# Kernel optimization log

Hardware: AMD Instinct MI355X
Metric: run time of the kernel (lower is better)

Reference implementation:

```python
import jax, jax.numpy as jnp
import numpy as np
import math

BS, T = 256, 128
DD, DT, DB = 128, 16, 32
DH, NH, DS = 256, 4, 64
DHN = DH * NH


def _lin(key, din, dout):
    kw, kb = jax.random.split(key)
    w = jax.random.normal(kw, (din, dout), jnp.float32) * 0.02
    bb = jax.random.normal(kb, (dout,), jnp.float32) * 0.02
    return w, bb


def setup_inputs() -> dict:
    key = jax.random.key(0)
    ks = jax.random.split(key, 16)
    inp = {
        "x": jax.random.normal(ks[0], (BS, T, DD), jnp.float32),
        "a": jax.random.normal(ks[1], (BS, T, DT), jnp.float32),
        "m": jnp.ones((BS, T, DD), jnp.float32),
        "b": jax.random.normal(ks[2], (BS, DB), jnp.float32),
        "eps": jax.random.normal(ks[3], (T - 1, BS, DS), jnp.float32),
    }
    inp["bk_w"], inp["bk_b"] = _lin(ks[4], DD + DB, DH)
    inp["bv_w"], inp["bv_b"] = _lin(ks[5], DD + DB, DHN)
    inp["q_w"], inp["q_b"] = _lin(ks[6], DD + DT, DHN)
    inp["v_w"], inp["v_b"] = _lin(ks[7], DD + DT, DHN)
    inp["hk_w"], inp["hk_b"] = _lin(ks[8], DS, DH)
    inp["hv_w"], inp["hv_b"] = _lin(ks[9], DS, DHN)
    inp["mu1_w"], inp["mu1_b"] = _lin(ks[10], DHN, DS)
    inp["sg1_w"], inp["sg1_b"] = _lin(ks[11], DHN, DS)
    inp["mut_w"], inp["mut_b"] = _lin(ks[12], DHN, DS)
    inp["sgt_w"], inp["sgt_b"] = _lin(ks[13], DHN, DS)
    return inp


def reference(x, a, m, b, eps,
              bk_w, bk_b, bv_w, bv_b, q_w, q_b, v_w, v_b,
              hk_w, hk_b, hv_w, hv_b,
              mu1_w, mu1_b, sg1_w, sg1_b, mut_w, mut_b, sgt_w, sgt_b):
    bs = x.shape[0]
    inp = jnp.concatenate([x[:, 1:, :], a[:, :-1, :]], -1)   # [bs, T-1, DD+DT]
    mask = (jnp.sum(m[:, 1:, :], -1) > 0.0).astype(x.dtype)  # [bs, T-1]

    q_inp = jax.nn.relu(inp @ q_w + q_b).reshape(bs, -1, DH, NH)  # [bs,T-1,DH,NH]
    v_inp = (inp @ v_w + v_b).reshape(bs, -1, DH, NH)

    scale = 1.0 / math.sqrt(DH)

    def attn(key_vec):  # key_vec: [bs, DH]
        scores = jnp.einsum('bd,btdh->bth', key_vec, q_inp) * scale
        scores = jnp.where(mask[..., None] > 0, scores, -1e9)
        p = jax.nn.softmax(scores, axis=1)                 # over time
        return jnp.einsum('bth,btdh->bdh', p, v_inp).reshape(bs, DHN)

    xb = jnp.concatenate([x[:, 0, :], b], -1)              # [bs, DD+DB]
    key1 = jax.nn.relu(xb @ bk_w + bk_b)
    val1 = xb @ bv_w + bv_b
    h1 = jax.nn.relu(0.5 * (attn(key1) + val1))
    mu1 = h1 @ mu1_w + mu1_b
    sg1 = jax.nn.softplus(h1 @ sg1_w + sg1_b)
    z1 = mu1 + sg1 * eps[0]

    def step(z_prev, e):
        keyt = jax.nn.relu(z_prev @ hk_w + hk_b)
        valt = z_prev @ hv_w + hv_b
        ht = jax.nn.relu(0.5 * (attn(keyt) + valt))
        mu = ht @ mut_w + mut_b
        sg = jax.nn.softplus(ht @ sgt_w + sgt_b)
        z = mu + sg * e
        return z, (z, mu, sg)

    _, (zs, mus, sgs) = jax.lax.scan(step, z1, eps[1:])
    Z = jnp.moveaxis(jnp.concatenate([z1[None], zs], 0), 0, 1)    # [bs, T-1, DS]
    MU = jnp.moveaxis(jnp.concatenate([mu1[None], mus], 0), 0, 1)
    SG = jnp.moveaxis(jnp.concatenate([sg1[None], sgs], 0), 0, 1)
    return Z, MU, SG
```

## Files before the change

### kernel.cpp

```cpp
#include <hip/hip_runtime.h>
#include <hip/hip_bf16.h>
#include <stdint.h>

#define BS   256
#define T_   128
#define TP   127
#define DD   128
#define DT   16
#define DB   32
#define DH   256
#define NH   4
#define DS   64
#define DHN  1024

#define OFFV (256u*127u*64u)

typedef __attribute__((ext_vector_type(8))) short short8v;
typedef __attribute__((ext_vector_type(4))) float f32x4;
typedef __attribute__((ext_vector_type(2))) unsigned int uint2v;

__device__ __forceinline__ float bf16lo(unsigned u){ return __uint_as_float(u << 16); }
__device__ __forceinline__ float bf16hi(unsigned u){ return __uint_as_float(u & 0xffff0000u); }
__device__ __forceinline__ unsigned short f2bf(float f){
  unsigned u = __float_as_uint(f);
  u += 0x7fffu + ((u >> 16) & 1u);
  return (unsigned short)(u >> 16);
}
__device__ __forceinline__ unsigned pk2(float lo, float hi){
  return (unsigned)f2bf(lo) | ((unsigned)f2bf(hi) << 16);
}
__device__ __forceinline__ float softplus_f(float x){
  return fmaxf(x, 0.f) + log1pf(__expf(-fabsf(x)));
}

__global__ __launch_bounds__(256) void pack_w_kernel(
    const float* __restrict__ hk_w, const float* __restrict__ hv_w,
    const float* __restrict__ mut_w, const float* __restrict__ sgt_w,
    unsigned* __restrict__ hkp, unsigned* __restrict__ hvp,
    unsigned* __restrict__ mutp, unsigned* __restrict__ sgtp)
{
  int i = blockIdx.x * 256 + threadIdx.x;
  if (i < 32*256) { int s2 = i >> 8, d = i & 255;
    hkp[i] = pk2(hk_w[(2*s2)*256 + d], hk_w[(2*s2+1)*256 + d]); }
  if (i < 32*1024) { int s2 = i >> 10, j = i & 1023;
    hvp[i] = pk2(hv_w[(2*s2)*1024 + j], hv_w[(2*s2+1)*1024 + j]); }
  if (i < 512*64) { int J2 = i >> 6, k = i & 63;
    mutp[i] = pk2(mut_w[(2*J2)*64 + k], mut_w[(2*J2+1)*64 + k]);
    sgtp[i] = pk2(sgt_w[(2*J2)*64 + k], sgt_w[(2*J2+1)*64 + k]); }
}

#define LDA 168

__global__ __launch_bounds__(256) void proj_kernel(
    const float* __restrict__ x, const float* __restrict__ a,
    const float* __restrict__ q_w, const float* __restrict__ q_b,
    const float* __restrict__ v_w, const float* __restrict__ v_b,
    uint2v* __restrict__ Qp4, unsigned* __restrict__ Vws)
{
  const int b    = blockIdx.x;
  const int tid  = threadIdx.x;
  const int lane = tid & 63;
  const int w    = tid >> 6;

  __shared__ __align__(16) unsigned short A_s[128 * LDA];
  __shared__ __align__(16) unsigned short BC_s[64 * LDA];

  for (int idx = tid; idx < 128 * DD; idx += 256) {
    int t = idx >> 7, k = idx & 127;
    float v = (t < TP) ? x[((size_t)b * T_ + 1 + t) * DD + k] : 0.f;
    A_s[t * LDA + k] = f2bf(v);
  }
  for (int idx = tid; idx < 128 * 40; idx += 256) {
    int t = idx / 40, kk = idx % 40;
    float v = (t < TP && kk < DT) ? a[((size_t)b * T_ + t) * DT + kk] : 0.f;
    A_s[t * LDA + 128 + kk] = f2bf(v);
  }
  __syncthreads();

  for (int nt = 0; nt < 32; ++nt) {
    const int n0 = nt * 64;
    const bool isQ = (n0 < DHN);
    const float* wsrc = isQ ? q_w : v_w;
    const float* bias = isQ ? q_b : v_b;
    const int nb = isQ ? n0 : (n0 - DHN);

    for (int idx = tid; idx < 160 * 64; idx += 256) {
      int k = idx >> 6, n = idx & 63;
      float v = (k < DD + DT) ? wsrc[(size_t)k * DHN + nb + n] : 0.f;
      BC_s[n * LDA + k] = f2bf(v);
    }
    __syncthreads();

    f32x4 acc[2][4];
#pragma unroll
    for (int mi = 0; mi < 2; ++mi)
#pragma unroll
      for (int ni = 0; ni < 4; ++ni) { f32x4 zz = {0.f,0.f,0.f,0.f}; acc[mi][ni] = zz; }
    const int mb = w * 32;
#pragma unroll
    for (int kc = 0; kc < 5; ++kc) {
      const int ko = kc * 32 + ((lane >> 4) << 3);
      short8v af[2], bf[4];
#pragma unroll
      for (int mi = 0; mi < 2; ++mi)
        af[mi] = *(const short8v*)&A_s[(mb + mi*16 + (lane & 15)) * LDA + ko];
#pragma unroll
      for (int ni = 0; ni < 4; ++ni)
        bf[ni] = *(const short8v*)&BC_s[(ni*16 + (lane & 15)) * LDA + ko];
#pragma unroll
      for (int mi = 0; mi < 2; ++mi)
#pragma unroll
        for (int ni = 0; ni < 4; ++ni)
          acc[mi][ni] = __builtin_amdgcn_mfma_f32_16x16x32_bf16(af[mi], bf[ni], acc[mi][ni], 0, 0, 0);
    }
    __syncthreads();

#pragma unroll
    for (int mi = 0; mi < 2; ++mi)
#pragma unroll
      for (int ni = 0; ni < 4; ++ni) {
        int cl = ni*16 + (lane & 15);
        float bb = bias[nb + cl];
#pragma unroll
        for (int q = 0; q < 4; ++q) {
          int t = mb + mi*16 + ((lane >> 4) << 2) + q;
          float vv = acc[mi][ni][q] + bb;
          if (isQ) vv = fmaxf(vv, 0.f);
          BC_s[t * 66 + cl] = f2bf(vv);
        }
      }
    __syncthreads();

    if (isQ) {
      for (int idx = tid; idx < 4 * 512; idx += 256) {
        int d4l = idx >> 9, r = idx & 511;
        int t = r >> 2, h = r & 3;
        const unsigned short* cr = &BC_s[t * 66 + d4l * 16 + h];
        uint2v u;
        u.x = (unsigned)cr[0] | ((unsigned)cr[4]  << 16);
        u.y = (unsigned)cr[8] | ((unsigned)cr[12] << 16);
        Qp4[((size_t)b * 64 + (n0 >> 4) + d4l) * 512 + r] = u;
      }
    } else {
      int c0 = (n0 - DHN) >> 1;
      for (int idx = tid; idx < 128 * 32; idx += 256) {
        int t = idx >> 5, c2 = idx & 31;
        const unsigned short* cr = &BC_s[t * 66 + c2 * 2];
        Vws[((size_t)b * 128 + t) * 512 + c0 + c2] = (unsigned)cr[0] | ((unsigned)cr[1] << 16);
      }
    }
    __syncthreads();
  }
}

__global__ __launch_bounds__(512) void recur_kernel(
    const float* __restrict__ x, const float* __restrict__ bvec,
    const float* __restrict__ m, const float* __restrict__ eps,
    const float* __restrict__ bk_w, const float* __restrict__ bk_b,
    const float* __restrict__ bv_w, const float* __restrict__ bv_b,
    const float* __restrict__ hk_b, const float* __restrict__ hv_b,
    const float* __restrict__ mu1_w, const float* __restrict__ mu1_b,
    const float* __restrict__ sg1_w, const float* __restrict__ sg1_b,
    const float* __restrict__ mut_b, const float* __restrict__ sgt_b,
    const unsigned* __restrict__ hkp, const unsigned* __restrict__ hvp,
    const unsigned* __restrict__ mutp, const unsigned* __restrict__ sgtp,
    const uint2v* __restrict__ Qp4, const unsigned* __restrict__ Vws,
    float* __restrict__ out)
{
  const int b    = blockIdx.x;
  const int tid  = threadIdx.x;
  const int lane = tid & 63;
  const int wv   = tid >> 6;

  __shared__ __align__(16) float key_s[DH];
  __shared__ __align__(16) float sc[512];
  __shared__ __align__(16) float p_s[128 * 4];
  __shared__ __align__(16) float val_s[DHN];
  __shared__ __align__(16) float ht_s[DHN];
  __shared__ __align__(16) float red[2 * 8 * 64];
  __shared__ __align__(16) float z_s[DS];
  __shared__ __align__(16) float xb[DD + DB];
  __shared__ float mask_s[128];
  __shared__ __align__(16) float hkb_s[DH];
  __shared__ __align__(16) float hvb_s[DHN];
  __shared__ float mtb_s[DS], stb_s[DS];

  if (tid < DD + DB) xb[tid] = (tid < DD) ? x[(size_t)b * T_ * DD + tid] : bvec[b * DB + (tid - DD)];
  if (tid >= 256 && tid < 512) hkb_s[tid - 256] = hk_b[tid - 256];
  for (int i = tid; i < DHN; i += 512) hvb_s[i] = hv_b[i];
  if (tid < DS) { mtb_s[tid] = mut_b[tid]; stb_s[tid] = sgt_b[tid]; }

  for (int t = wv; t < TP; t += 8) {
    const float* mr = m + ((size_t)b * T_ + 1 + t) * DD;
    float s = mr[lane] + mr[lane + 64];
    for (int o = 1; o < 64; o <<= 1) s += __shfl_xor(s, o);
    if (lane == 0) mask_s[t] = (s > 0.f) ? 1.f : 0.f;
  }
  if (tid == 0) mask_s[127] = 0.f;
  __syncthreads();

  const uint2v*   qp = Qp4 + (size_t)b * 64 * 512 + tid;
  const unsigned* vp = Vws + (size_t)b * 128 * 512 + tid;
  const int h0 = (tid & 1) * 2;

  auto attn_phase = [&]() {
    float acc0 = 0.f, acc1 = 0.f;
#pragma unroll 8
    for (int d4 = 0; d4 < 64; ++d4) {
      uint2v q = __builtin_nontemporal_load(qp + (size_t)d4 * 512);
      float4 kk = *(const float4*)&key_s[d4 * 4];
      acc0 = fmaf(bf16lo(q.x), kk.x, acc0);
      acc1 = fmaf(bf16hi(q.x), kk.y, acc1);
      acc0 = fmaf(bf16lo(q.y), kk.z, acc0);
      acc1 = fmaf(bf16hi(q.y), kk.w, acc1);
    }
    {
      int t = tid >> 2;
      float s = acc0 + acc1;
      sc[tid] = (mask_s[t] > 0.f) ? s * 0.0625f : -1e9f;
    }
    __syncthreads();
    if (tid < 256) {
      int h = wv, l = lane;
      float v1 = sc[l * 4 + h];
      float v2 = (l + 64 < TP) ? sc[(l + 64) * 4 + h] : -3.0e38f;
      float mm = fmaxf(v1, v2);
      for (int o = 1; o < 64; o <<= 1) mm = fmaxf(mm, __shfl_xor(mm, o));
      float e1 = __expf(v1 - mm);
      float e2 = (l + 64 < TP) ? __expf(v2 - mm) : 0.f;
      float ssum = e1 + e2;
      for (int o = 1; o < 64; o <<= 1) ssum += __shfl_xor(ssum, o);
      float inv = 1.f / ssum;
      p_s[l * 4 + h] = e1 * inv;
      if (l + 64 < TP) p_s[(l + 64) * 4 + h] = e2 * inv;
    }
    __syncthreads();
    float a0 = 0.f, a1 = 0.f;
#pragma unroll 4
    for (int t2 = 0; t2 < TP; ++t2) {
      unsigned v = __builtin_nontemporal_load(vp + (size_t)t2 * 512);
      float2 pp = *(const float2*)&p_s[t2 * 4 + h0];
      a0 = fmaf(pp.x, bf16lo(v), a0);
      a1 = fmaf(pp.y, bf16hi(v), a1);
    }
    int j = tid * 2;
    ht_s[j]     = fmaxf(0.5f * (a0 + val_s[j]), 0.f);
    ht_s[j + 1] = fmaxf(0.5f * (a1 + val_s[j + 1]), 0.f);
    __syncthreads();
  };

  if (tid < 256) {
    float acc = bk_b[tid];
    for (int s = 0; s < DD + DB; ++s) acc = fmaf(xb[s], bk_w[s * DH + tid], acc);
    key_s[tid] = fmaxf(acc, 0.f);
  } else {
    int c = tid - 256;
    float a0 = bv_b[c], a1 = bv_b[c + 256], a2 = bv_b[c + 512], a3 = bv_b[c + 768];
    for (int s = 0; s < DD + DB; ++s) {
      float xs = xb[s];
      const float* r = bv_w + (size_t)s * DHN + c;
      a0 = fmaf(xs, r[0], a0);   a1 = fmaf(xs, r[256], a1);
      a2 = fmaf(xs, r[512], a2); a3 = fmaf(xs, r[768], a3);
    }
    val_s[c] = a0; val_s[c + 256] = a1; val_s[c + 512] = a2; val_s[c + 768] = a3;
  }
  __syncthreads();

  attn_phase();

  {
    int k = tid & 63, g = tid >> 6;
    float am = 0.f, as_ = 0.f;
    for (int jl = 0; jl < 128; ++jl) {
      int j = g * 128 + jl;
      float hj = ht_s[j];
      am  = fmaf(hj, mu1_w[(size_t)j * 64 + k], am);
      as_ = fmaf(hj, sg1_w[(size_t)j * 64 + k], as_);
    }
    red[g * 64 + k] = am; red[512 + g * 64 + k] = as_;
  }
  __syncthreads();
  if (tid < 64) {
    float mu = mu1_b[tid], sl = sg1_b[tid];
    for (int g = 0; g < 8; ++g) { mu += red[g * 64 + tid]; sl += red[512 + g * 64 + tid]; }
    float sg = softplus_f(sl);
    float z  = fmaf(sg, eps[(size_t)b * 64 + tid], mu);
    size_t o0 = ((size_t)b * TP + 0) * 64 + tid;
    out[o0] = z; out[OFFV + o0] = mu; out[2ull * OFFV + o0] = sg;
    z_s[tid] = z;
  }
  __syncthreads();

  for (int st = 1; st < TP; ++st) {
    if (tid < 256) {
      float acc = hkb_s[tid];
#pragma unroll 8
      for (int s2 = 0; s2 < 32; ++s2) {
        unsigned wq = hkp[s2 * 256 + tid];
        float2 zz = *(const float2*)&z_s[s2 * 2];
        acc = fmaf(zz.x, bf16lo(wq), acc);
        acc = fmaf(zz.y, bf16hi(wq), acc);
      }
      key_s[tid] = fmaxf(acc, 0.f);
    } else {
      int c = tid - 256;
      float a0 = hvb_s[c], a1 = hvb_s[c + 256], a2 = hvb_s[c + 512], a3 = hvb_s[c + 768];
#pragma unroll 4
      for (int s2 = 0; s2 < 32; ++s2) {
        float2 zz = *(const float2*)&z_s[s2 * 2];
        unsigned w0 = hvp[s2 * 1024 + c];
        unsigned w1 = hvp[s2 * 1024 + c + 256];
        unsigned w2 = hvp[s2 * 1024 + c + 512];
        unsigned w3 = hvp[s2 * 1024 + c + 768];
        a0 = fmaf(zz.x, bf16lo(w0), a0); a0 = fmaf(zz.y, bf16hi(w0), a0);
        a1 = fmaf(zz.x, bf16lo(w1), a1); a1 = fmaf(zz.y, bf16hi(w1), a1);
        a2 = fmaf(zz.x, bf16lo(w2), a2); a2 = fmaf(zz.y, bf16hi(w2), a2);
        a3 = fmaf(zz.x, bf16lo(w3), a3); a3 = fmaf(zz.y, bf16hi(w3), a3);
      }
      val_s[c] = a0; val_s[c + 256] = a1; val_s[c + 512] = a2; val_s[c + 768] = a3;
    }
    __syncthreads();

    attn_phase();

    {
      int k = tid & 63, g = tid >> 6;
      float am0 = 0.f, am1 = 0.f, as0 = 0.f, as1 = 0.f;
#pragma unroll 4
      for (int j2 = 0; j2 < 64; ++j2) {
        int J2 = g * 64 + j2;
        float2 hh = *(const float2*)&ht_s[J2 * 2];
        unsigned wm = mutp[J2 * 64 + k];
        unsigned ws = sgtp[J2 * 64 + k];
        am0 = fmaf(hh.x, bf16lo(wm), am0);
        am1 = fmaf(hh.y, bf16hi(wm), am1);
        as0 = fmaf(hh.x, bf16lo(ws), as0);
        as1 = fmaf(hh.y, bf16hi(ws), as1);
      }
      red[g * 64 + k] = am0 + am1; red[512 + g * 64 + k] = as0 + as1;
    }
    __syncthreads();
    if (tid < 64) {
      float mu = mtb_s[tid], sl = stb_s[tid];
      for (int g = 0; g < 8; ++g) { mu += red[g * 64 + tid]; sl += red[512 + g * 64 + tid]; }
      float sg = softplus_f(sl);
      float z  = fmaf(sg, eps[((size_t)st * BS + b) * 64 + tid], mu);
      size_t o0 = ((size_t)b * TP + st) * 64 + tid;
      out[o0] = z; out[OFFV + o0] = mu; out[2ull * OFFV + o0] = sg;
      z_s[tid] = z;
    }
    __syncthreads();
  }
}

extern "C" void kernel_launch(void* const* d_in, const int* in_sizes, int n_in,
                              void* d_out, int out_size, void* d_ws, size_t ws_size,
                              hipStream_t stream) {
  const float* x    = (const float*)d_in[0];
  const float* a    = (const float*)d_in[1];
  const float* m    = (const float*)d_in[2];
  const float* bvec = (const float*)d_in[3];
  const float* eps  = (const float*)d_in[4];
  const float* bk_w = (const float*)d_in[5];
  const float* bk_b = (const float*)d_in[6];
  const float* bv_w = (const float*)d_in[7];
  const float* bv_b = (const float*)d_in[8];
  const float* q_w  = (const float*)d_in[9];
  const float* q_b  = (const float*)d_in[10];
  const float* v_w  = (const float*)d_in[11];
  const float* v_b  = (const float*)d_in[12];
  const float* hk_w = (const float*)d_in[13];
  const float* hk_b = (const float*)d_in[14];
  const float* hv_w = (const float*)d_in[15];
  const float* hv_b = (const float*)d_in[16];
  const float* mu1_w= (const float*)d_in[17];
  const float* mu1_b= (const float*)d_in[18];
  const float* sg1_w= (const float*)d_in[19];
  const float* sg1_b= (const float*)d_in[20];
  const float* mut_w= (const float*)d_in[21];
  const float* mut_b= (const float*)d_in[22];
  const float* sgt_w= (const float*)d_in[23];
  const float* sgt_b= (const float*)d_in[24];

  char* ws = (char*)d_ws;
  uint2v*   Qp4  = (uint2v*)ws;
  unsigned* Vws  = (unsigned*)(ws + (64ull << 20));
  unsigned* hkp  = (unsigned*)(ws + (128ull << 20));
  unsigned* hvp  = hkp + 32 * 256;
  unsigned* mutp = hvp + 32 * 1024;
  unsigned* sgtp = mutp + 512 * 64;

  pack_w_kernel<<<dim3(128), dim3(256), 0, stream>>>(hk_w, hv_w, mut_w, sgt_w,
                                                     hkp, hvp, mutp, sgtp);
  proj_kernel<<<dim3(256), dim3(256), 0, stream>>>(x, a, q_w, q_b, v_w, v_b, Qp4, Vws);
  recur_kernel<<<dim3(256), dim3(512), 0, stream>>>(x, bvec, m, eps,
      bk_w, bk_b, bv_w, bv_b, hk_b, hv_b,
      mu1_w, mu1_b, sg1_w, sg1_b, mut_b, sgt_b,
      hkp, hvp, mutp, sgtp, Qp4, Vws, (float*)d_out);
}
```

Measured before the change: 6.137 ms.

## Keep per-batch Q and V attention operands register-resident, compressing V to fp8

```diff
diff --git a/kernel.cpp b/kernel.cpp
--- a/kernel.cpp
+++ b/kernel.cpp
@@ -17,6 +17,7 @@
 
 typedef __attribute__((ext_vector_type(8))) short short8v;
 typedef __attribute__((ext_vector_type(4))) float f32x4;
+typedef __attribute__((ext_vector_type(2))) float f32x2;
 typedef __attribute__((ext_vector_type(2))) unsigned int uint2v;
 
 __device__ __forceinline__ float bf16lo(unsigned u){ return __uint_as_float(u << 16); }
@@ -174,7 +175,7 @@
 
   __shared__ __align__(16) float key_s[DH];
   __shared__ __align__(16) float sc[512];
-  __shared__ __align__(16) float p_s[128 * 4];
+  __shared__ __align__(16) float ppair[2][128][2];
   __shared__ __align__(16) float val_s[DHN];
   __shared__ __align__(16) float ht_s[DHN];
   __shared__ __align__(16) float red[2 * 8 * 64];
@@ -189,6 +190,10 @@
   if (tid >= 256 && tid < 512) hkb_s[tid - 256] = hk_b[tid - 256];
   for (int i = tid; i < DHN; i += 512) hvb_s[i] = hv_b[i];
   if (tid < DS) { mtb_s[tid] = mut_b[tid]; stb_s[tid] = sgt_b[tid]; }
+  if (tid < 128) {
+    ppair[0][tid][0] = 0.f; ppair[0][tid][1] = 0.f;
+    ppair[1][tid][0] = 0.f; ppair[1][tid][1] = 0.f;
+  }
 
   for (int t = wv; t < TP; t += 8) {
     const float* mr = m + ((size_t)b * T_ + 1 + t) * DD;
@@ -197,28 +202,41 @@
     if (lane == 0) mask_s[t] = (s > 0.f) ? 1.f : 0.f;
   }
   if (tid == 0) mask_s[127] = 0.f;
+
+  uint2v qreg[64];
+  {
+    const uint2v* qp = Qp4 + (size_t)b * 64 * 512 + tid;
+#pragma unroll
+    for (int d4 = 0; d4 < 64; ++d4) qreg[d4] = qp[(size_t)d4 * 512];
+  }
+  unsigned vreg[64];
+  {
+    const unsigned* vp = Vws + (size_t)b * 128 * 512 + tid;
+#pragma unroll
+    for (int i = 0; i < 64; ++i) {
+      unsigned w0 = vp[(size_t)(2*i)   * 512];
+      unsigned w1 = vp[(size_t)(2*i+1) * 512];
+      int pk = __builtin_amdgcn_cvt_pk_fp8_f32(bf16lo(w0), bf16hi(w0), 0, false);
+      pk     = __builtin_amdgcn_cvt_pk_fp8_f32(bf16lo(w1), bf16hi(w1), pk, true);
+      vreg[i] = (unsigned)pk;
+    }
+  }
   __syncthreads();
 
-  const uint2v*   qp = Qp4 + (size_t)b * 64 * 512 + tid;
-  const unsigned* vp = Vws + (size_t)b * 128 * 512 + tid;
-  const int h0 = (tid & 1) * 2;
+  const int hp = tid & 1;
 
   auto attn_phase = [&]() {
     float acc0 = 0.f, acc1 = 0.f;
-#pragma unroll 8
+#pragma unroll
     for (int d4 = 0; d4 < 64; ++d4) {
-      uint2v q = __builtin_nontemporal_load(qp + (size_t)d4 * 512);
       float4 kk = *(const float4*)&key_s[d4 * 4];
+      uint2v q = qreg[d4];
       acc0 = fmaf(bf16lo(q.x), kk.x, acc0);
       acc1 = fmaf(bf16hi(q.x), kk.y, acc1);
       acc0 = fmaf(bf16lo(q.y), kk.z, acc0);
       acc1 = fmaf(bf16hi(q.y), kk.w, acc1);
     }
-    {
-      int t = tid >> 2;
-      float s = acc0 + acc1;
-      sc[tid] = (mask_s[t] > 0.f) ? s * 0.0625f : -1e9f;
-    }
+    sc[tid] = (mask_s[tid >> 2] > 0.f) ? (acc0 + acc1) * 0.0625f : -1e9f;
     __syncthreads();
     if (tid < 256) {
       int h = wv, l = lane;
@@ -231,17 +249,18 @@
       float ssum = e1 + e2;
       for (int o = 1; o < 64; o <<= 1) ssum += __shfl_xor(ssum, o);
       float inv = 1.f / ssum;
-      p_s[l * 4 + h] = e1 * inv;
-      if (l + 64 < TP) p_s[(l + 64) * 4 + h] = e2 * inv;
+      ppair[h >> 1][l][h & 1] = e1 * inv;
+      if (l + 64 < TP) ppair[h >> 1][l + 64][h & 1] = e2 * inv;
     }
     __syncthreads();
     float a0 = 0.f, a1 = 0.f;
-#pragma unroll 4
-    for (int t2 = 0; t2 < TP; ++t2) {
-      unsigned v = __builtin_nontemporal_load(vp + (size_t)t2 * 512);
-      float2 pp = *(const float2*)&p_s[t2 * 4 + h0];
-      a0 = fmaf(pp.x, bf16lo(v), a0);
-      a1 = fmaf(pp.y, bf16hi(v), a1);
+#pragma unroll
+    for (int i = 0; i < 64; ++i) {
+      float4 pp = *(const float4*)&ppair[hp][2 * i][0];
+      f32x2 v01 = __builtin_amdgcn_cvt_pk_f32_fp8(vreg[i], false);
+      f32x2 v23 = __builtin_amdgcn_cvt_pk_f32_fp8(vreg[i], true);
+      a0 = fmaf(pp.x, v01.x, a0); a1 = fmaf(pp.y, v01.y, a1);
+      a0 = fmaf(pp.z, v23.x, a0); a1 = fmaf(pp.w, v23.y, a1);
     }
     int j = tid * 2;
     ht_s[j]     = fmaxf(0.5f * (a0 + val_s[j]), 0.f);
```

Measured after the change: 9.002 ms. +46.7%, slower.
